# Kernel tuning notes

Hardware: AMD Instinct MI355X
Metric: run time of the kernel (lower is better)

The kernel has to match this reference:

```python
import jax, jax.numpy as jnp
import numpy as np

B, S, D = 2, 2048, 2048
H = 16
Q_LORA, KV_LORA = 1536, 512
ROPE_DIM, NOPE_DIM, V_DIM = 64, 64, 128
Q_HEAD_DIM = NOPE_DIM + ROPE_DIM  # 128
ROPE_THETA, ROPE_RATIO = 10000.0, 1.0


def setup_inputs() -> dict:
    key = jax.random.key(0)
    ks = jax.random.split(key, 6)
    std = 0.02
    return {
        "hidden_states": jax.random.normal(ks[0], (B, S, D), jnp.float32),
        "Wqa": jax.random.normal(ks[1], (D, Q_LORA), jnp.float32) * std,
        "Wqb": jax.random.normal(ks[2], (Q_LORA, H * Q_HEAD_DIM), jnp.float32) * std,
        "Wkva": jax.random.normal(ks[3], (D, KV_LORA + ROPE_DIM), jnp.float32) * std,
        "Wkvb": jax.random.normal(ks[4], (KV_LORA, H * (NOPE_DIM + V_DIM)), jnp.float32) * std,
        "Wo": jax.random.normal(ks[5], (H * V_DIM, D), jnp.float32) * std,
    }


def _rope_tables(seq_len):
    half = ROPE_DIM // 2
    inv_freq = ROPE_RATIO / (ROPE_THETA ** (jnp.arange(half, dtype=jnp.float32) * 2.0 / ROPE_DIM))
    freqs = jnp.arange(seq_len, dtype=jnp.float32)[:, None] * inv_freq[None, :]  # [S, half]
    return jnp.cos(freqs), jnp.sin(freqs)


def _apply_rope(x, cos, sin):
    # interleaved even/odd rotation, matches torch stack+flatten
    x_even = x[..., 0::2]
    x_odd = x[..., 1::2]
    r_even = x_even * cos - x_odd * sin
    r_odd = x_odd * cos + x_even * sin
    return jnp.stack([r_even, r_odd], axis=-1).reshape(x.shape)


def reference(hidden_states, Wqa, Wqb, Wkva, Wkvb, Wo):
    b, s, _ = hidden_states.shape
    scale = Q_HEAD_DIM ** -0.5

    # query compression path
    q_latent = hidden_states @ Wqa                             # [B,S,Q_LORA]
    q = (q_latent @ Wqb).reshape(b, s, H, Q_HEAD_DIM)
    q = jnp.transpose(q, (0, 2, 1, 3))                          # [B,H,S,q_head_dim]
    q_nope, q_pe = q[..., :NOPE_DIM], q[..., NOPE_DIM:]

    # kv compression
    kv_comp = hidden_states @ Wkva                              # [B,S,KV_LORA+ROPE]
    c_kv, k_pe = kv_comp[..., :KV_LORA], kv_comp[..., KV_LORA:]

    cos, sin = _rope_tables(s)                                  # [S, ROPE_DIM//2]
    q_pe = _apply_rope(q_pe, cos, sin)                          # [B,H,S,ROPE]
    k_pe = _apply_rope(k_pe, cos, sin)                          # [B,S,ROPE]

    # kv decompression
    kv = (c_kv @ Wkvb).reshape(b, s, H, NOPE_DIM + V_DIM)
    kv = jnp.transpose(kv, (0, 2, 1, 3))                        # [B,H,S,nope+v]
    k_nope, v = kv[..., :NOPE_DIM], kv[..., NOPE_DIM:]

    k_pe_b = jnp.broadcast_to(k_pe[:, None], (b, H, s, ROPE_DIM))
    q_full = jnp.concatenate([q_nope, q_pe], axis=-1)           # [B,H,S,128]
    k_full = jnp.concatenate([k_nope, k_pe_b], axis=-1)         # [B,H,S,128]

    scores = jnp.einsum('bhqd,bhkd->bhqk', q_full, k_full) * scale
    causal = jnp.tril(jnp.ones((s, s), dtype=bool))
    scores = jnp.where(causal[None, None], scores, jnp.finfo(scores.dtype).min)
    probs = jax.nn.softmax(scores, axis=-1)
    attn = jnp.einsum('bhqk,bhkd->bhqd', probs, v)              # [B,H,S,V_DIM]

    out = jnp.transpose(attn, (0, 2, 1, 3)).reshape(b, s, H * V_DIM)
    return out @ Wo                                             # [B,S,D]
```

## Files before the change

### kernel.cpp

```cpp
#include <hip/hip_runtime.h>
#include <hip/hip_bf16.h>
#include <cstdint>
#include <cstddef>

typedef __bf16 bf16_t;
typedef __attribute__((ext_vector_type(8))) __bf16 bf16x8;
typedef __attribute__((ext_vector_type(4))) float f32x4;

#define S_ 2048
#define H_ 16
#define NTOK 4096

__device__ __forceinline__ f32x4 mfma16x16(bf16x8 a, bf16x8 b, f32x4 c) {
  return __builtin_amdgcn_mfma_f32_16x16x32_bf16(a, b, c, 0, 0, 0);
}
__device__ __forceinline__ bf16x8 load8(const bf16_t* p) {
  return *reinterpret_cast<const bf16x8*>(p);
}
__device__ __forceinline__ void load_lds16(const void* g, void* l) {
  __builtin_amdgcn_global_load_lds(
      (const __attribute__((address_space(1))) uint32_t*)g,
      (__attribute__((address_space(3))) uint32_t*)l, 16, 0, 0);
}


__global__ void cast_bf16_k(const float* __restrict__ in, bf16_t* __restrict__ out, int n) {
  int idx = blockIdx.x * 256 + threadIdx.x;
  int i4 = idx * 4;
  if (i4 >= n) return;
  float4 v = *reinterpret_cast<const float4*>(in + i4);
  out[i4 + 0] = (bf16_t)v.x;
  out[i4 + 1] = (bf16_t)v.y;
  out[i4 + 2] = (bf16_t)v.z;
  out[i4 + 3] = (bf16_t)v.w;
}

struct TDesc {
  const float* src;
  bf16_t* dst;
  int K, Nsrc, bxc, off;
};
struct TDesc5 {
  TDesc d[5];
};

__global__ void transpose_cast_multi_k(TDesc5 ds) {
  __shared__ float tile[32][33];
  const int bid = blockIdx.x;
  int i = 0;
#pragma unroll
  for (int j = 1; j < 5; ++j)
    if (bid >= ds.d[j].off) i = j;
  const float* __restrict__ in = ds.d[i].src;
  bf16_t* __restrict__ out = ds.d[i].dst;
  const int K = ds.d[i].K, Nsrc = ds.d[i].Nsrc;
  const int local = bid - ds.d[i].off;
  const int n0 = (local % ds.d[i].bxc) * 32;
  const int k0 = (local / ds.d[i].bxc) * 32;
  int tx = threadIdx.x & 31, ty = threadIdx.x >> 5;
#pragma unroll
  for (int r = 0; r < 4; ++r) {
    int k = k0 + ty + r * 8, n = n0 + tx;
    tile[ty + r * 8][tx] = (n < Nsrc) ? in[(size_t)k * Nsrc + n] : 0.0f;
  }
  __syncthreads();
#pragma unroll
  for (int r = 0; r < 4; ++r) {
    int n = n0 + ty + r * 8, k = k0 + tx;
    out[(size_t)n * K + k] = (bf16_t)tile[tx][ty + r * 8];
  }
}

__global__ void transpose_v_k(const bf16_t* __restrict__ kv, bf16_t* __restrict__ vT) {
  __shared__ bf16_t tile[32][33];
  int bh = blockIdx.z;
  int b = bh >> 4, h = bh & 15;
  int s0 = blockIdx.x * 32, d0 = blockIdx.y * 32;
  int tx = threadIdx.x & 31, ty = threadIdx.x >> 5;
#pragma unroll
  for (int i = 0; i < 4; ++i) {
    int s = s0 + ty + i * 8;
    tile[ty + i * 8][tx] = kv[(size_t)(b * S_ + s) * 3072 + h * 192 + 64 + d0 + tx];
  }
  __syncthreads();
#pragma unroll
  for (int i = 0; i < 4; ++i) {
    int d = d0 + ty + i * 8;
    vT[((size_t)bh * 128 + d) * 2048 + s0 + tx] = tile[tx][ty + i * 8];
  }
}

__global__ void rope_tables_k(float* __restrict__ cosT, float* __restrict__ sinT) {
  int idx = blockIdx.x * 256 + threadIdx.x;
  if (idx >= S_ * 32) return;
  int s = idx >> 5, i = idx & 31;
  float inv = powf(10000.0f, -(2.0f * (float)i) / 64.0f);
  float fr = (float)s * inv;
  cosT[idx] = cosf(fr);
  sinT[idx] = sinf(fr);
}

__global__ void rope_apply_k(bf16_t* __restrict__ buf, const float* __restrict__ cosT,
                             const float* __restrict__ sinT, int ld, int nh, int hstride, int off) {
  int idx = blockIdx.x * 256 + threadIdx.x;
  int total = NTOK * nh * 32;
  if (idx >= total) return;
  int i = idx & 31;
  int h = (idx >> 5) % nh;
  int t = idx / (32 * nh);
  int s = t & (S_ - 1);
  float c = cosT[s * 32 + i], sn = sinT[s * 32 + i];
  bf16_t* p = buf + (size_t)t * ld + off + h * hstride + 2 * i;
  float xe = (float)p[0], xo = (float)p[1];
  p[0] = (bf16_t)(xe * c - xo * sn);
  p[1] = (bf16_t)(xo * c + xe * sn);
}


template <int OUT_F32>
__global__ __launch_bounds__(256) void gemm_bf16(const bf16_t* __restrict__ A, int lda,
                                                 const bf16_t* __restrict__ Bt,
                                                 void* __restrict__ Cv, int M, int N, int K,
                                                 float scale) {
  __shared__ alignas(16) bf16_t Al[128 * 32];
  __shared__ alignas(16) bf16_t Bl[128 * 32];
  const int tid = threadIdx.x;
  const int wid = tid >> 6, lane = tid & 63;
  const int m0 = blockIdx.y * 128, n0 = blockIdx.x * 128;
  const int wm = (wid >> 1) * 64, wn = (wid & 1) * 64;

  f32x4 acc[4][4] = {};

  const int srow = wid * 32 + (lane >> 2);
  const int scol = (lane & 3) * 8;
  const bf16_t* ag0 = A + (size_t)(m0 + srow) * lda + scol;
  const bf16_t* ag1 = A + (size_t)(m0 + srow + 16) * lda + scol;
  const bf16_t* bg0 = Bt + (size_t)(n0 + srow) * K + scol;
  const bf16_t* bg1 = Bt + (size_t)(n0 + srow + 16) * K + scol;
  bf16_t* al0 = &Al[wid * 1024];
  bf16_t* al1 = &Al[wid * 1024 + 512];
  bf16_t* bl0 = &Bl[wid * 1024];
  bf16_t* bl1 = &Bl[wid * 1024 + 512];

  const int lr = lane & 15, lk = (lane >> 4) * 8;

  for (int k0 = 0; k0 < K; k0 += 32) {
    load_lds16(ag0 + k0, al0);
    load_lds16(ag1 + k0, al1);
    load_lds16(bg0 + k0, bl0);
    load_lds16(bg1 + k0, bl1);
    __syncthreads();
    bf16x8 af[4], bfr[4];
#pragma unroll
    for (int i = 0; i < 4; ++i) {
      af[i] = load8(&Al[(wm + i * 16 + lr) * 32 + lk]);
      bfr[i] = load8(&Bl[(wn + i * 16 + lr) * 32 + lk]);
    }
#pragma unroll
    for (int i = 0; i < 4; ++i)
#pragma unroll
      for (int j = 0; j < 4; ++j) acc[i][j] = mfma16x16(af[i], bfr[j], acc[i][j]);
    __syncthreads();
  }

  const int lg = lane >> 4;
  if (OUT_F32) {
    float* C = (float*)Cv;
#pragma unroll
    for (int i = 0; i < 4; ++i)
#pragma unroll
      for (int j = 0; j < 4; ++j)
#pragma unroll
        for (int r = 0; r < 4; ++r) {
          int row = m0 + wm + i * 16 + lg * 4 + r;
          int col = n0 + wn + j * 16 + lr;
          C[(size_t)row * N + col] = acc[i][j][r] * scale;
        }
  } else {
    bf16_t* C = (bf16_t*)Cv;
#pragma unroll
    for (int i = 0; i < 4; ++i)
#pragma unroll
      for (int j = 0; j < 4; ++j)
#pragma unroll
        for (int r = 0; r < 4; ++r) {
          int row = m0 + wm + i * 16 + lg * 4 + r;
          int col = n0 + wn + j * 16 + lr;
          C[(size_t)row * N + col] = (bf16_t)(acc[i][j][r] * scale);
        }
  }
}

__global__ __launch_bounds__(256) void attn_fused(const bf16_t* __restrict__ q,
                                                  const bf16_t* __restrict__ kv,
                                                  const bf16_t* __restrict__ lat,
                                                  const bf16_t* __restrict__ vT,
                                                  bf16_t* __restrict__ out) {
  __shared__ alignas(16) bf16_t Kn[64 * 64];
  __shared__ alignas(16) bf16_t Kp[64 * 64];
  __shared__ alignas(16) bf16_t Vt[128 * 64];
  __shared__ alignas(16) bf16_t Pl[4][16 * 64];
  const int tid = threadIdx.x, wid = tid >> 6, lane = tid & 63;
  const int bid = blockIdx.x;
  const int g = bid >> 8;
  const int x = (bid >> 5) & 7;
  const int bh = bid & 31;
  const int qt = (g & 1) ? (24 - g * 8 + x) : (31 - g * 8 - x);
  const int b = bh >> 4, h = bh & 15;
  const int tokb = b * S_;
  const int lr = lane & 15, lg = lane >> 4;
  const int srow8 = lane >> 3, c8 = lane & 7;
  const int swz8 = c8 ^ srow8;
  bf16_t* Pw = &Pl[wid][0];

  bf16x8 ones;
#pragma unroll
  for (int j = 0; j < 8; ++j) ones[j] = (bf16_t)1.0f;

  bf16x8 qf[4];
  {
    const int qrow = qt * 64 + wid * 16 + lr;
    const bf16_t* qp = q + (size_t)(tokb + qrow) * 2048 + h * 128 + lg * 8;
#pragma unroll
    for (int ds = 0; ds < 4; ++ds) qf[ds] = load8(qp + ds * 32);
  }

  f32x4 o[8] = {};
  f32x4 o8 = {};
  float mrow[4] = {-1e30f, -1e30f, -1e30f, -1e30f};

  for (int t = 0; t <= qt; ++t) {
    const int kb = t * 64;
#pragma unroll
    for (int rr = 0; rr < 2; ++rr) {
      const int r0 = wid * 16 + rr * 8;
      const size_t tk = (size_t)(tokb + kb + r0 + srow8);
      load_lds16(kv + tk * 3072 + h * 192 + (swz8 << 3), &Kn[r0 * 64]);
      load_lds16(lat + tk * 2176 + 2048 + (swz8 << 3), &Kp[r0 * 64]);
    }
#pragma unroll
    for (int rr = 0; rr < 4; ++rr) {
      const int r0 = wid * 32 + rr * 8;
      load_lds16(vT + ((size_t)bh * 128 + r0 + srow8) * 2048 + kb + (swz8 << 3), &Vt[r0 * 64]);
    }
    __syncthreads();

    f32x4 s[4];
    __builtin_amdgcn_s_setprio(1);
#pragma unroll
    for (int kt = 0; kt < 4; ++kt) {
      const int row = kt * 16 + lr;
      const int e = lr & 7;
      bf16x8 kf0 = load8(&Kn[row * 64 + ((lg ^ e) << 3)]);
      bf16x8 kf1 = load8(&Kn[row * 64 + (((lg + 4) ^ e) << 3)]);
      bf16x8 kf2 = load8(&Kp[row * 64 + ((lg ^ e) << 3)]);
      bf16x8 kf3 = load8(&Kp[row * 64 + (((lg + 4) ^ e) << 3)]);
      f32x4 acc = {0.f, 0.f, 0.f, 0.f};
      acc = mfma16x16(qf[0], kf0, acc);
      acc = mfma16x16(qf[1], kf1, acc);
      acc = mfma16x16(qf[2], kf2, acc);
      acc = mfma16x16(qf[3], kf3, acc);
      s[kt] = acc;
    }
    __builtin_amdgcn_s_setprio(0);

    if (t == qt) {
#pragma unroll
      for (int kt = 0; kt < 4; ++kt) {
        const int key = kb + kt * 16 + lr;
#pragma unroll
        for (int r = 0; r < 4; ++r) {
          const int qr = qt * 64 + wid * 16 + lg * 4 + r;
          if (key > qr) s[kt][r] = -1e30f;
        }
      }
    }

    float tm[4];
#pragma unroll
    for (int r = 0; r < 4; ++r) {
      float mx = fmaxf(fmaxf(s[0][r], s[1][r]), fmaxf(s[2][r], s[3][r]));
      mx = fmaxf(mx, __shfl_xor(mx, 1));
      mx = fmaxf(mx, __shfl_xor(mx, 2));
      mx = fmaxf(mx, __shfl_xor(mx, 4));
      mx = fmaxf(mx, __shfl_xor(mx, 8));
      tm[r] = mx;
    }
    float need = fmaxf(fmaxf(tm[0] - mrow[0], tm[1] - mrow[1]),
                       fmaxf(tm[2] - mrow[2], tm[3] - mrow[3]));
    if (!__all(need <= 8.0f)) {
#pragma unroll
      for (int r = 0; r < 4; ++r) {
        float mn = fmaxf(mrow[r], tm[r]);
        float corr = exp2f(mrow[r] - mn);
        mrow[r] = mn;
        o8[r] *= corr;
#pragma unroll
        for (int n = 0; n < 8; ++n) o[n][r] *= corr;
      }
    }
#pragma unroll
    for (int kt = 0; kt < 4; ++kt)
#pragma unroll
      for (int r = 0; r < 4; ++r) s[kt][r] = exp2f(s[kt][r] - mrow[r]);

#pragma unroll
    for (int kt = 0; kt < 4; ++kt)
#pragma unroll
      for (int r = 0; r < 4; ++r) {
        const int qrow = lg * 4 + r;
        const int key = kt * 16 + lr;
        Pw[qrow * 64 + ((((key >> 3) ^ (qrow & 7)) << 3) | (key & 7))] = (bf16_t)s[kt][r];
      }

    __builtin_amdgcn_s_setprio(1);
#pragma unroll
    for (int ks = 0; ks < 2; ++ks) {
      const int e = lr & 7;
      bf16x8 pa = load8(&Pw[lr * 64 + (((ks * 4 + lg) ^ e) << 3)]);
#pragma unroll
      for (int n = 0; n < 8; ++n) {
        bf16x8 vb = load8(&Vt[(n * 16 + lr) * 64 + (((ks * 4 + lg) ^ e) << 3)]);
        o[n] = mfma16x16(pa, vb, o[n]);
      }
      o8 = mfma16x16(pa, ones, o8);
    }
    __builtin_amdgcn_s_setprio(0);
    __syncthreads();
  }

  float linv[4];
#pragma unroll
  for (int r = 0; r < 4; ++r) linv[r] = __builtin_amdgcn_rcpf(o8[r]);
#pragma unroll
  for (int n = 0; n < 8; ++n)
#pragma unroll
    for (int r = 0; r < 4; ++r) {
      const int qr = qt * 64 + wid * 16 + lg * 4 + r;
      out[(size_t)(tokb + qr) * 2048 + h * 128 + n * 16 + lr] = (bf16_t)(o[n][r] * linv[r]);
    }
}


extern "C" void kernel_launch(void* const* d_in, const int* in_sizes, int n_in, void* d_out,
                              int out_size, void* d_ws, size_t ws_size, hipStream_t stream) {
  const float* hs = (const float*)d_in[0];
  const float* Wqa = (const float*)d_in[1];
  const float* Wqb = (const float*)d_in[2];
  const float* Wkva = (const float*)d_in[3];
  const float* Wkvb = (const float*)d_in[4];
  const float* Wo = (const float*)d_in[5];
  float* out = (float*)d_out;

  char* ws = (char*)d_ws;
  size_t off = 0;
  auto alloc = [&](size_t bytes) {
    void* p = ws + off;
    off += (bytes + 255) & ~(size_t)255;
    return p;
  };
  bf16_t* hsb = (bf16_t*)alloc((size_t)NTOK * 2048 * 2);
  bf16_t* W1t = (bf16_t*)alloc((size_t)2176 * 2048 * 2);
  bf16_t* Wqbt = (bf16_t*)alloc((size_t)2048 * 1536 * 2);
  bf16_t* Wkvbt = (bf16_t*)alloc((size_t)3072 * 512 * 2);
  bf16_t* Wot = (bf16_t*)alloc((size_t)2048 * 2048 * 2);
  bf16_t* lat = (bf16_t*)alloc((size_t)NTOK * 2176 * 2);
  bf16_t* qb = (bf16_t*)alloc((size_t)NTOK * 2048 * 2);
  bf16_t* kvb = (bf16_t*)alloc((size_t)NTOK * 3072 * 2);
  bf16_t* attn = (bf16_t*)alloc((size_t)NTOK * 2048 * 2);
  bf16_t* vT = (bf16_t*)alloc((size_t)32 * 128 * 2048 * 2);
  float* cosT = (float*)alloc((size_t)S_ * 32 * 4);
  float* sinT = (float*)alloc((size_t)S_ * 32 * 4);

  cast_bf16_k<<<(NTOK * 2048 / 4 + 255) / 256, 256, 0, stream>>>(hs, hsb, NTOK * 2048);
  {
    TDesc5 ds;
    int o0 = 0;
    auto add = [&](int i, const float* src, bf16_t* dst, int K, int Nsrc, int Nout) {
      int bxc = Nout / 32, cnt = bxc * (K / 32);
      ds.d[i] = TDesc{src, dst, K, Nsrc, bxc, o0};
      o0 += cnt;
    };
    add(0, Wqa, W1t, 2048, 1536, 1536);
    add(1, Wkva, W1t + (size_t)1536 * 2048, 2048, 576, 640);
    add(2, Wqb, Wqbt, 1536, 2048, 2048);
    add(3, Wkvb, Wkvbt, 512, 3072, 3072);
    add(4, Wo, Wot, 2048, 2048, 2048);
    transpose_cast_multi_k<<<o0, 256, 0, stream>>>(ds);
  }
  rope_tables_k<<<(S_ * 32 + 255) / 256, 256, 0, stream>>>(cosT, sinT);

  gemm_bf16<0><<<dim3(2176 / 128, NTOK / 128), 256, 0, stream>>>(hsb, 2048, W1t, lat, NTOK, 2176,
                                                                 2048, 1.0f);
  rope_apply_k<<<(NTOK * 32 + 255) / 256, 256, 0, stream>>>(lat, cosT, sinT, 2176, 1, 0, 2048);
  const float scale = 0.08838834764831845f * 1.4426950408889634f;
  gemm_bf16<0><<<dim3(2048 / 128, NTOK / 128), 256, 0, stream>>>(lat, 2176, Wqbt, qb, NTOK, 2048,
                                                                 1536, scale);
  rope_apply_k<<<(NTOK * 16 * 32 + 255) / 256, 256, 0, stream>>>(qb, cosT, sinT, 2048, 16, 128, 64);
  gemm_bf16<0><<<dim3(3072 / 128, NTOK / 128), 256, 0, stream>>>(lat + 1536, 2176, Wkvbt, kvb, NTOK,
                                                                 3072, 512, 1.0f);
  transpose_v_k<<<dim3(64, 4, 32), 256, 0, stream>>>(kvb, vT);
  attn_fused<<<dim3(1024), 256, 0, stream>>>(qb, kvb, lat, vT, attn);
  gemm_bf16<1><<<dim3(2048 / 128, NTOK / 128), 256, 0, stream>>>(attn, 2048, Wot, out, NTOK, 2048,
                                                                 2048, 1.0f);
}
```

Measured before the change: 309.1 us.

## Fuse RoPE and V-transpose into GEMM epilogues and merge q/kv GEMMs

Applies RoPE inside the epilogues of the latent and query GEMMs using lane shuffles. The two decompression GEMMs now run as one launch. The kv decompression weight is permuted so k_nope and V land in contiguous column ranges, and V is written pre-transposed straight from the epilogue. This removes the separate rope_apply and transpose_v kernels, their extra HBM round-trips, and several launches. The cost is strided 8-byte vT stores and per-element cos/sin loads in the epilogues.

```diff
diff --git a/kernel.cpp b/kernel.cpp
--- a/kernel.cpp
+++ b/kernel.cpp
@@ -4,6 +4,7 @@
 #include <cstddef>
 
 typedef __bf16 bf16_t;
+typedef __attribute__((ext_vector_type(4))) __bf16 bf16x4;
 typedef __attribute__((ext_vector_type(8))) __bf16 bf16x8;
 typedef __attribute__((ext_vector_type(4))) float f32x4;
 
@@ -35,10 +36,20 @@
   out[i4 + 3] = (bf16_t)v.w;
 }
 
+__global__ void rope_tables_k(float* __restrict__ cosT, float* __restrict__ sinT) {
+  int idx = blockIdx.x * 256 + threadIdx.x;
+  if (idx >= S_ * 32) return;
+  int s = idx >> 5, i = idx & 31;
+  float inv = powf(10000.0f, -(2.0f * (float)i) / 64.0f);
+  float fr = (float)s * inv;
+  cosT[idx] = cosf(fr);
+  sinT[idx] = sinf(fr);
+}
+
 struct TDesc {
   const float* src;
   bf16_t* dst;
-  int K, Nsrc, bxc, off;
+  int K, Nsrc, bxc, off, perm;
 };
 struct TDesc5 {
   TDesc d[5];
@@ -57,10 +68,15 @@
   const int local = bid - ds.d[i].off;
   const int n0 = (local % ds.d[i].bxc) * 32;
   const int k0 = (local / ds.d[i].bxc) * 32;
+  int srcn0 = n0;
+  if (ds.d[i].perm) {
+    srcn0 = (n0 < 1024) ? ((n0 >> 6) * 192 + (n0 & 63))
+                        : (((n0 - 1024) >> 7) * 192 + 64 + ((n0 - 1024) & 127));
+  }
   int tx = threadIdx.x & 31, ty = threadIdx.x >> 5;
 #pragma unroll
   for (int r = 0; r < 4; ++r) {
-    int k = k0 + ty + r * 8, n = n0 + tx;
+    int k = k0 + ty + r * 8, n = srcn0 + tx;
     tile[ty + r * 8][tx] = (n < Nsrc) ? in[(size_t)k * Nsrc + n] : 0.0f;
   }
   __syncthreads();
@@ -71,66 +87,12 @@
   }
 }
 
-__global__ void transpose_v_k(const bf16_t* __restrict__ kv, bf16_t* __restrict__ vT) {
-  __shared__ bf16_t tile[32][33];
-  int bh = blockIdx.z;
-  int b = bh >> 4, h = bh & 15;
-  int s0 = blockIdx.x * 32, d0 = blockIdx.y * 32;
-  int tx = threadIdx.x & 31, ty = threadIdx.x >> 5;
-#pragma unroll
-  for (int i = 0; i < 4; ++i) {
-    int s = s0 + ty + i * 8;
-    tile[ty + i * 8][tx] = kv[(size_t)(b * S_ + s) * 3072 + h * 192 + 64 + d0 + tx];
-  }
-  __syncthreads();
-#pragma unroll
-  for (int i = 0; i < 4; ++i) {
-    int d = d0 + ty + i * 8;
-    vT[((size_t)bh * 128 + d) * 2048 + s0 + tx] = tile[tx][ty + i * 8];
-  }
-}
-
-__global__ void rope_tables_k(float* __restrict__ cosT, float* __restrict__ sinT) {
-  int idx = blockIdx.x * 256 + threadIdx.x;
-  if (idx >= S_ * 32) return;
-  int s = idx >> 5, i = idx & 31;
-  float inv = powf(10000.0f, -(2.0f * (float)i) / 64.0f);
-  float fr = (float)s * inv;
-  cosT[idx] = cosf(fr);
-  sinT[idx] = sinf(fr);
-}
-
-__global__ void rope_apply_k(bf16_t* __restrict__ buf, const float* __restrict__ cosT,
-                             const float* __restrict__ sinT, int ld, int nh, int hstride, int off) {
-  int idx = blockIdx.x * 256 + threadIdx.x;
-  int total = NTOK * nh * 32;
-  if (idx >= total) return;
-  int i = idx & 31;
-  int h = (idx >> 5) % nh;
-  int t = idx / (32 * nh);
-  int s = t & (S_ - 1);
-  float c = cosT[s * 32 + i], sn = sinT[s * 32 + i];
-  bf16_t* p = buf + (size_t)t * ld + off + h * hstride + 2 * i;
-  float xe = (float)p[0], xo = (float)p[1];
-  p[0] = (bf16_t)(xe * c - xo * sn);
-  p[1] = (bf16_t)(xo * c + xe * sn);
-}
-
-
-template <int OUT_F32>
-__global__ __launch_bounds__(256) void gemm_bf16(const bf16_t* __restrict__ A, int lda,
-                                                 const bf16_t* __restrict__ Bt,
-                                                 void* __restrict__ Cv, int M, int N, int K,
-                                                 float scale) {
-  __shared__ alignas(16) bf16_t Al[128 * 32];
-  __shared__ alignas(16) bf16_t Bl[128 * 32];
-  const int tid = threadIdx.x;
+
+__device__ __forceinline__ void gemm_loop(const bf16_t* __restrict__ A, int lda,
+                                          const bf16_t* __restrict__ Bt, int K, int m0, int n0,
+                                          int tid, bf16_t* Al, bf16_t* Bl, f32x4 (&acc)[4][4]) {
   const int wid = tid >> 6, lane = tid & 63;
-  const int m0 = blockIdx.y * 128, n0 = blockIdx.x * 128;
   const int wm = (wid >> 1) * 64, wn = (wid & 1) * 64;
-
-  f32x4 acc[4][4] = {};
-
   const int srow = wid * 32 + (lane >> 2);
   const int scol = (lane & 3) * 8;
   const bf16_t* ag0 = A + (size_t)(m0 + srow) * lda + scol;
@@ -141,7 +103,6 @@
   bf16_t* al1 = &Al[wid * 1024 + 512];
   bf16_t* bl0 = &Bl[wid * 1024];
   bf16_t* bl1 = &Bl[wid * 1024 + 512];
-
   const int lr = lane & 15, lk = (lane >> 4) * 8;
 
   for (int k0 = 0; k0 < K; k0 += 32) {
@@ -162,37 +123,163 @@
       for (int j = 0; j < 4; ++j) acc[i][j] = mfma16x16(af[i], bfr[j], acc[i][j]);
     __syncthreads();
   }
-
-  const int lg = lane >> 4;
-  if (OUT_F32) {
-    float* C = (float*)Cv;
+}
+
+
+__global__ __launch_bounds__(256) void gemm_lat_k(const bf16_t* __restrict__ A,
+                                                  const bf16_t* __restrict__ Bt,
+                                                  bf16_t* __restrict__ C,
+                                                  const float* __restrict__ cosT,
+                                                  const float* __restrict__ sinT) {
+  __shared__ alignas(16) bf16_t Al[128 * 32];
+  __shared__ alignas(16) bf16_t Bl[128 * 32];
+  const int tid = threadIdx.x;
+  const int m0 = blockIdx.y * 128, n0 = blockIdx.x * 128;
+  f32x4 acc[4][4] = {};
+  gemm_loop(A, 2048, Bt, 2048, m0, n0, tid, Al, Bl, acc);
+
+  const int wid = tid >> 6, lane = tid & 63;
+  const int wm = (wid >> 1) * 64, wn = (wid & 1) * 64;
+  const int lr = lane & 15, lg = lane >> 4;
+  const bool rope = (n0 == 2048) && (wn == 0);
+  const int ir_base = lr >> 1;
+  const bool odd = lane & 1;
+#pragma unroll
+  for (int i = 0; i < 4; ++i)
+#pragma unroll
+    for (int j = 0; j < 4; ++j) {
+      float v4[4];
+#pragma unroll
+      for (int r = 0; r < 4; ++r) v4[r] = acc[i][j][r];
+      if (rope) {
+        const int ir = j * 8 + ir_base;
+#pragma unroll
+        for (int r = 0; r < 4; ++r) {
+          const int srow_ = (m0 + wm + i * 16 + lg * 4 + r) & (S_ - 1);
+          float c = cosT[srow_ * 32 + ir], sn = sinT[srow_ * 32 + ir];
+          float partner = __shfl_xor(v4[r], 1);
+          v4[r] = odd ? (v4[r] * c + partner * sn) : (v4[r] * c - partner * sn);
+        }
+      }
+#pragma unroll
+      for (int r = 0; r < 4; ++r) {
+        int row = m0 + wm + i * 16 + lg * 4 + r;
+        int col = n0 + wn + j * 16 + lr;
+        C[(size_t)row * 2176 + col] = (bf16_t)v4[r];
+      }
+    }
+}
+
+
+__global__ __launch_bounds__(256) void gemm_qkv_k(const bf16_t* __restrict__ lat,
+                                                  const bf16_t* __restrict__ Wqbt,
+                                                  const bf16_t* __restrict__ Wkvbt,
+                                                  bf16_t* __restrict__ qb,
+                                                  bf16_t* __restrict__ knb,
+                                                  bf16_t* __restrict__ vT,
+                                                  const float* __restrict__ cosT,
+                                                  const float* __restrict__ sinT, float qscale) {
+  __shared__ alignas(16) bf16_t Al[128 * 32];
+  __shared__ alignas(16) bf16_t Bl[128 * 32];
+  const int tid = threadIdx.x;
+  const int bid = blockIdx.x;
+  const int wid = tid >> 6, lane = tid & 63;
+  const int wm = (wid >> 1) * 64, wn = (wid & 1) * 64;
+  const int lr = lane & 15, lg = lane >> 4;
+  f32x4 acc[4][4] = {};
+
+  if (bid < 512) {
+    const int m0 = (bid >> 4) * 128, n0 = (bid & 15) * 128;
+    gemm_loop(lat, 2176, Wqbt, 1536, m0, n0, tid, Al, Bl, acc);
+    const bool rope = (wn == 64);
+    const int ir_base = lr >> 1;
+    const bool odd = lane & 1;
 #pragma unroll
     for (int i = 0; i < 4; ++i)
 #pragma unroll
-      for (int j = 0; j < 4; ++j)
+      for (int j = 0; j < 4; ++j) {
+        float v4[4];
+#pragma unroll
+        for (int r = 0; r < 4; ++r) v4[r] = acc[i][j][r] * qscale;
+        if (rope) {
+          const int ir = j * 8 + ir_base;
+#pragma unroll
+          for (int r = 0; r < 4; ++r) {
+            const int srow_ = (m0 + wm + i * 16 + lg * 4 + r) & (S_ - 1);
+            float c = cosT[srow_ * 32 + ir], sn = sinT[srow_ * 32 + ir];
+            float partner = __shfl_xor(v4[r], 1);
+            v4[r] = odd ? (v4[r] * c + partner * sn) : (v4[r] * c - partner * sn);
+          }
+        }
 #pragma unroll
         for (int r = 0; r < 4; ++r) {
           int row = m0 + wm + i * 16 + lg * 4 + r;
           int col = n0 + wn + j * 16 + lr;
-          C[(size_t)row * N + col] = acc[i][j][r] * scale;
+          qb[(size_t)row * 2048 + col] = (bf16_t)v4[r];
         }
+      }
   } else {
-    bf16_t* C = (bf16_t*)Cv;
-#pragma unroll
-    for (int i = 0; i < 4; ++i)
-#pragma unroll
-      for (int j = 0; j < 4; ++j)
-#pragma unroll
-        for (int r = 0; r < 4; ++r) {
-          int row = m0 + wm + i * 16 + lg * 4 + r;
-          int col = n0 + wn + j * 16 + lr;
-          C[(size_t)row * N + col] = (bf16_t)(acc[i][j][r] * scale);
+    const int b2 = bid - 512;
+    const int m0 = (b2 / 24) * 128, n0 = (b2 % 24) * 128;
+    gemm_loop(lat + 1536, 2176, Wkvbt, 512, m0, n0, tid, Al, Bl, acc);
+    if (n0 < 1024) {
+#pragma unroll
+      for (int i = 0; i < 4; ++i)
+#pragma unroll
+        for (int j = 0; j < 4; ++j)
+#pragma unroll
+          for (int r = 0; r < 4; ++r) {
+            int row = m0 + wm + i * 16 + lg * 4 + r;
+            int col = n0 + wn + j * 16 + lr;
+            knb[(size_t)row * 1024 + col] = (bf16_t)acc[i][j][r];
+          }
+    } else {
+#pragma unroll
+      for (int i = 0; i < 4; ++i) {
+        const int row0 = m0 + wm + i * 16 + lg * 4;
+        const int bb = row0 >> 11;
+        const int s0 = row0 & (S_ - 1);
+#pragma unroll
+        for (int j = 0; j < 4; ++j) {
+          const int idx = n0 + wn + j * 16 + lr - 1024;
+          const int h = idx >> 7, d = idx & 127;
+          bf16x4 pk;
+#pragma unroll
+          for (int r = 0; r < 4; ++r) pk[r] = (bf16_t)acc[i][j][r];
+          *reinterpret_cast<bf16x4*>(&vT[((size_t)(bb * 16 + h) * 128 + d) * 2048 + s0]) = pk;
         }
-  }
+      }
+    }
+  }
+}
+
+
+__global__ __launch_bounds__(256) void gemm_out_k(const bf16_t* __restrict__ A,
+                                                  const bf16_t* __restrict__ Bt,
+                                                  float* __restrict__ C) {
+  __shared__ alignas(16) bf16_t Al[128 * 32];
+  __shared__ alignas(16) bf16_t Bl[128 * 32];
+  const int tid = threadIdx.x;
+  const int m0 = blockIdx.y * 128, n0 = blockIdx.x * 128;
+  f32x4 acc[4][4] = {};
+  gemm_loop(A, 2048, Bt, 2048, m0, n0, tid, Al, Bl, acc);
+  const int wid = tid >> 6, lane = tid & 63;
+  const int wm = (wid >> 1) * 64, wn = (wid & 1) * 64;
+  const int lr = lane & 15, lg = lane >> 4;
+#pragma unroll
+  for (int i = 0; i < 4; ++i)
+#pragma unroll
+    for (int j = 0; j < 4; ++j)
+#pragma unroll
+      for (int r = 0; r < 4; ++r) {
+        int row = m0 + wm + i * 16 + lg * 4 + r;
+        int col = n0 + wn + j * 16 + lr;
+        C[(size_t)row * 2048 + col] = acc[i][j][r];
+      }
 }
 
 __global__ __launch_bounds__(256) void attn_fused(const bf16_t* __restrict__ q,
-                                                  const bf16_t* __restrict__ kv,
+                                                  const bf16_t* __restrict__ knb,
                                                   const bf16_t* __restrict__ lat,
                                                   const bf16_t* __restrict__ vT,
                                                   bf16_t* __restrict__ out) {
@@ -235,7 +322,7 @@
     for (int rr = 0; rr < 2; ++rr) {
       const int r0 = wid * 16 + rr * 8;
       const size_t tk = (size_t)(tokb + kb + r0 + srow8);
-      load_lds16(kv + tk * 3072 + h * 192 + (swz8 << 3), &Kn[r0 * 64]);
+      load_lds16(knb + tk * 1024 + h * 64 + (swz8 << 3), &Kn[r0 * 64]);
       load_lds16(lat + tk * 2176 + 2048 + (swz8 << 3), &Kp[r0 * 64]);
     }
 #pragma unroll
@@ -366,41 +453,33 @@
   bf16_t* Wot = (bf16_t*)alloc((size_t)2048 * 2048 * 2);
   bf16_t* lat = (bf16_t*)alloc((size_t)NTOK * 2176 * 2);
   bf16_t* qb = (bf16_t*)alloc((size_t)NTOK * 2048 * 2);
-  bf16_t* kvb = (bf16_t*)alloc((size_t)NTOK * 3072 * 2);
+  bf16_t* knb = (bf16_t*)alloc((size_t)NTOK * 1024 * 2);
   bf16_t* attn = (bf16_t*)alloc((size_t)NTOK * 2048 * 2);
   bf16_t* vT = (bf16_t*)alloc((size_t)32 * 128 * 2048 * 2);
   float* cosT = (float*)alloc((size_t)S_ * 32 * 4);
   float* sinT = (float*)alloc((size_t)S_ * 32 * 4);
 
   cast_bf16_k<<<(NTOK * 2048 / 4 + 255) / 256, 256, 0, stream>>>(hs, hsb, NTOK * 2048);
+  rope_tables_k<<<(S_ * 32 + 255) / 256, 256, 0, stream>>>(cosT, sinT);
   {
     TDesc5 ds;
     int o0 = 0;
-    auto add = [&](int i, const float* src, bf16_t* dst, int K, int Nsrc, int Nout) {
+    auto add = [&](int i, const float* src, bf16_t* dst, int K, int Nsrc, int Nout, int perm) {
       int bxc = Nout / 32, cnt = bxc * (K / 32);
-      ds.d[i] = TDesc{src, dst, K, Nsrc, bxc, o0};
+      ds.d[i] = TDesc{src, dst, K, Nsrc, bxc, o0, perm};
       o0 += cnt;
     };
-    add(0, Wqa, W1t, 2048, 1536, 1536);
-    add(1, Wkva, W1t + (size_t)1536 * 2048, 2048, 576, 640);
-    add(2, Wqb, Wqbt, 1536, 2048, 2048);
-    add(3, Wkvb, Wkvbt, 512, 3072, 3072);
-    add(4, Wo, Wot, 2048, 2048, 2048);
+    add(0, Wqa, W1t, 2048, 1536, 1536, 0);
+    add(1, Wkva, W1t + (size_t)1536 * 2048, 2048, 576, 640, 0);
+    add(2, Wqb, Wqbt, 1536, 2048, 2048, 0);
+    add(3, Wkvb, Wkvbt, 512, 3072, 3072, 1);
+    add(4, Wo, Wot, 2048, 2048, 2048, 0);
     transpose_cast_multi_k<<<o0, 256, 0, stream>>>(ds);
   }
-  rope_tables_k<<<(S_ * 32 + 255) / 256, 256, 0, stream>>>(cosT, sinT);
-
-  gemm_bf16<0><<<dim3(2176 / 128, NTOK / 128), 256, 0, stream>>>(hsb, 2048, W1t, lat, NTOK, 2176,
-                                                                 2048, 1.0f);
-  rope_apply_k<<<(NTOK * 32 + 255) / 256, 256, 0, stream>>>(lat, cosT, sinT, 2176, 1, 0, 2048);
+
+  gemm_lat_k<<<dim3(17, 32), 256, 0, stream>>>(hsb, W1t, lat, cosT, sinT);
   const float scale = 0.08838834764831845f * 1.4426950408889634f;
-  gemm_bf16<0><<<dim3(2048 / 128, NTOK / 128), 256, 0, stream>>>(lat, 2176, Wqbt, qb, NTOK, 2048,
-                                                                 1536, scale);
-  rope_apply_k<<<(NTOK * 16 * 32 + 255) / 256, 256, 0, stream>>>(qb, cosT, sinT, 2048, 16, 128, 64);
-  gemm_bf16<0><<<dim3(3072 / 128, NTOK / 128), 256, 0, stream>>>(lat + 1536, 2176, Wkvbt, kvb, NTOK,
-                                                                 3072, 512, 1.0f);
-  transpose_v_k<<<dim3(64, 4, 32), 256, 0, stream>>>(kvb, vT);
-  attn_fused<<<dim3(1024), 256, 0, stream>>>(qb, kvb, lat, vT, attn);
-  gemm_bf16<1><<<dim3(2048 / 128, NTOK / 128), 256, 0, stream>>>(attn, 2048, Wot, out, NTOK, 2048,
-                                                                 2048, 1.0f);
-}
+  gemm_qkv_k<<<dim3(1280), 256, 0, stream>>>(lat, Wqbt, Wkvbt, qb, knb, vT, cosT, sinT, scale);
+  attn_fused<<<dim3(1024), 256, 0, stream>>>(qb, knb, lat, vT, attn);
+  gemm_out_k<<<dim3(16, 32), 256, 0, stream>>>(attn, Wot, out);
+}
```

Measured after the change: 306.7 us. About the same (-0.8%).
